# Optimization experiments

Hardware: AMD Instinct MI355X
Metric: run time of the kernel (lower is better)

The kernel has to match this reference:

```python
import jax, jax.numpy as jnp
import numpy as np

B, CIN, COUT, H, W = 4, 256, 256, 64, 64
K, G = 3, 4
PAD = (K - 1) // 2


def setup_inputs() -> dict:
    key = jax.random.key(0)
    k0, k1, k2, k3 = jax.random.split(key, 4)
    x = jax.random.normal(k0, (B, CIN, H, W), jnp.float32)
    y = jax.random.normal(k1, (B, 2, H, W), jnp.float32)
    # conv_offset: 1x1 conv, no bias, init std=0.1 (normal_init)
    w_offset = jax.random.normal(k2, (G * 2 * K * K, 2, 1, 1), jnp.float32) * 0.1
    # DeformConv2d weight, no bias, init std=0.01
    w_deform = jax.random.normal(k3, (COUT, CIN, K, K), jnp.float32) * 0.01
    return {"x": x, "y": y, "w_offset": w_offset, "w_deform": w_deform}


def _deform_conv(x, offset, weight):
    """DCN v1: stride 1, dilation 1, zero padding PAD, deform_groups=G, groups=1."""
    KK = K * K
    # mmcv offset layout: [B, G*2*KK, H, W] -> per group, per kernel pos, (dy, dx)
    off = offset.reshape(B, G, KK, 2, H, W)
    dy, dx = off[:, :, :, 0], off[:, :, :, 1]            # [B,G,KK,H,W]
    ii, jj = jnp.meshgrid(jnp.arange(K), jnp.arange(K), indexing="ij")
    ky = ii.reshape(KK).astype(x.dtype)                  # kernel row offsets
    kx = jj.reshape(KK).astype(x.dtype)                  # kernel col offsets
    base_y = jnp.arange(H, dtype=x.dtype)[None, :, None] - PAD + ky[:, None, None]  # [KK,H,1]
    base_x = jnp.arange(W, dtype=x.dtype)[None, None, :] - PAD + kx[:, None, None]  # [KK,1,W]
    yc = dy + base_y                                     # [B,G,KK,H,W]
    xc = dx + base_x

    Cg = CIN // G
    xg = x.reshape(B, G, Cg, H, W)

    def sample(xg1, yc1, xc1):
        # xg1 [Cg,H,W]; yc1/xc1 [KK,H,W] -> bilinear sample with zero padding
        y0 = jnp.floor(yc1)
        x0 = jnp.floor(xc1)
        wy = yc1 - y0
        wx = xc1 - x0
        y0i = y0.astype(jnp.int32)
        x0i = x0.astype(jnp.int32)

        def gather(yi, xi):
            valid = (yi >= 0) & (yi < H) & (xi >= 0) & (xi < W)
            v = xg1[:, jnp.clip(yi, 0, H - 1), jnp.clip(xi, 0, W - 1)]  # [Cg,KK,H,W]
            return v * valid[None].astype(xg1.dtype)

        v00 = gather(y0i, x0i)
        v01 = gather(y0i, x0i + 1)
        v10 = gather(y0i + 1, x0i)
        v11 = gather(y0i + 1, x0i + 1)
        return (v00 * (1 - wy) * (1 - wx) + v01 * (1 - wy) * wx
                + v10 * wy * (1 - wx) + v11 * wy * wx)

    sampled = jax.vmap(jax.vmap(sample))(xg, yc, xc)     # [B,G,Cg,KK,H,W]
    sampled = sampled.reshape(B, CIN, KK, H, W)
    wflat = weight.reshape(COUT, CIN, KK)
    return jnp.einsum("bckhw,ock->bohw", sampled, wflat)  # [B,COUT,H,W]


def reference(x, y, w_offset, w_deform):
    # offset = conv_offset(y.detach()), a 1x1 conv without bias
    y_det = jax.lax.stop_gradient(y)
    offset = jnp.einsum("bihw,oi->bohw", y_det, w_offset[:, :, 0, 0])
    out = _deform_conv(x, offset, w_deform)
    return jax.nn.relu(out)
```

## Files before the change

### kernel.cpp

```cpp
#include <hip/hip_runtime.h>
#include <cstddef>

#define B_    4
#define CIN_  256
#define COUT_ 256
#define H_    64
#define W_    64
#define KK_   9
#define G_    4
#define PAD_  1
#define TP    32

typedef short bf16x8 __attribute__((ext_vector_type(8)));
typedef float f32x4  __attribute__((ext_vector_type(4)));
typedef __attribute__((address_space(1))) const unsigned int* gptr_t;
typedef __attribute__((address_space(3))) unsigned int*       lptr_t;

__device__ __forceinline__ unsigned short f2bf(float v) {
    unsigned int u = __float_as_uint(v);
    u += 0x7fffu + ((u >> 16) & 1u);
    return (unsigned short)(u >> 16);
}
__device__ __forceinline__ float f_lo(unsigned int u) { return __uint_as_float(u << 16); }
__device__ __forceinline__ float f_hi(unsigned int u) { return __uint_as_float(u & 0xffff0000u); }

__global__ __launch_bounds__(256) void xt_kernel(const float* __restrict__ x,
                                                 unsigned short* __restrict__ xT) {
    __shared__ unsigned short s[128][66];
    const int tid   = threadIdx.x;
    const int bh    = blockIdx.x >> 1;
    const int chalf = blockIdx.x & 1;
    const size_t src_base = ((size_t)(bh >> 6) * CIN_ + chalf * 128) * (H_ * W_) + (bh & 63) * W_;
    #pragma unroll 4
    for (int k = 0; k < 32; ++k) {
        int i = k * 256 + tid;
        int c = i >> 6, w = i & 63;
        s[c][w] = f2bf(x[src_base + (size_t)c * (H_ * W_) + w]);
    }
    __syncthreads();
    #pragma unroll 4
    for (int k = 0; k < 16; ++k) {
        int j  = k * 256 + tid;
        int c2 = (j & 63) * 2, w = j >> 6;
        unsigned int lo = s[c2][w], hi = s[c2 + 1][w];
        *(unsigned int*)(xT + ((size_t)bh * 64 + w) * 256 + chalf * 128 + c2) = lo | (hi << 16);
    }
}

__global__ __launch_bounds__(256) void wt_kernel(const float* __restrict__ w,
                                                 unsigned short* __restrict__ wb) {
    int idx = blockIdx.x * 256 + threadIdx.x;
    int e   = idx & 7;
    int pos = (idx >> 3) & 7;
    int o   = (idx >> 6) & 255;
    int t   = idx >> 14;
    int g   = t / 9, kk = t - g * 9;
    int j   = pos ^ (o & 7);
    int c   = g * 64 + j * 8 + e;
    wb[idx] = f2bf(w[(o * CIN_ + c) * KK_ + kk]);
}

__global__ __launch_bounds__(256, 2) void dcn_kernel(
    const unsigned short* __restrict__ xT, const float* __restrict__ y,
    const float* __restrict__ w_off, const unsigned short* __restrict__ wb,
    float* __restrict__ out)
{
    __shared__ unsigned short s_W[COUT_ * 64];
    __shared__ unsigned short s_S[TP * 64];
    __shared__ float          s_off[72 * TP];

    const int tid = threadIdx.x;
    const int bid = blockIdx.x;
    const int xcd = bid & 7, loc = bid >> 3;
    const int b   = xcd >> 1;
    const int h   = (xcd & 1) * 32 + (loc >> 1);
    const int w0  = (loc & 1) * TP;

    for (int i = tid; i < 72 * TP; i += 256) {
        int p = i & 31, ch = i >> 5;
        float yv0 = y[((b * 2 + 0) * H_ + h) * W_ + w0 + p];
        float yv1 = y[((b * 2 + 1) * H_ + h) * W_ + w0 + p];
        s_off[i] = fmaf(yv0, w_off[ch * 2], yv1 * w_off[ch * 2 + 1]);
    }

    const int sp   = tid & 31;
    const int c8   = tid >> 5;
    const int lane = tid & 63, wave = tid >> 6;
    const int nt   = wave & 1, mh = wave >> 1;
    const int l15  = lane & 15, kq = lane >> 4, sw = l15 & 7;

    f32x4 acc[8];
    #pragma unroll
    for (int i = 0; i < 8; ++i) acc[i] = (f32x4){0.f, 0.f, 0.f, 0.f};

    for (int g = 0; g < G_; ++g) {
        for (int kk = 0; kk < KK_; ++kk) {
            const int step = g * KK_ + kk;
            __syncthreads();

            const unsigned short* src = wb + (size_t)step * 16384;
            #pragma unroll
            for (int j = 0; j < 8; ++j) {
                const int off = (j * 256 + tid) * 8;
                __builtin_amdgcn_global_load_lds((gptr_t)(src + off),
                                                 (lptr_t)(s_W + off), 16, 0, 0);
            }

            {
                const int   chy = step * 2;
                const float dy  = s_off[chy * 32 + sp];
                const float dx  = s_off[chy * 32 + 32 + sp];
                const float yc  = (float)(h + (kk / 3) - PAD_) + dy;
                const float xc  = (float)(w0 + sp + (kk % 3) - PAD_) + dx;
                const float yf  = floorf(yc), xf = floorf(xc);
                const float wy  = yc - yf,    wx = xc - xf;
                const int   yi  = (int)yf,    xi = (int)xf;
                float w00 = (1.f - wy) * (1.f - wx);
                float w01 = (1.f - wy) * wx;
                float w10 = wy * (1.f - wx);
                float w11 = wy * wx;
                const bool y0ok = (yi >= 0) & (yi < H_);
                const bool y1ok = (yi >= -1) & (yi < H_ - 1);
                const bool x0ok = (xi >= 0) & (xi < W_);
                const bool x1ok = (xi >= -1) & (xi < W_ - 1);
                w00 = (y0ok & x0ok) ? w00 : 0.f;
                w01 = (y0ok & x1ok) ? w01 : 0.f;
                w10 = (y1ok & x0ok) ? w10 : 0.f;
                w11 = (y1ok & x1ok) ? w11 : 0.f;
                const int y0c = min(max(yi, 0), H_ - 1);
                const int y1c = min(max(yi + 1, 0), H_ - 1);
                const int x0c = min(max(xi, 0), W_ - 1);
                const int x1c = min(max(xi + 1, 0), W_ - 1);
                const unsigned short* xb = xT + g * 64 + c8 * 8;
                const size_t bb = (size_t)b * (H_ * W_ * 256);
                const uint4 A = *(const uint4*)(xb + bb + ((size_t)y0c * W_ + x0c) * 256);
                const uint4 Bv= *(const uint4*)(xb + bb + ((size_t)y0c * W_ + x1c) * 256);
                const uint4 C = *(const uint4*)(xb + bb + ((size_t)y1c * W_ + x0c) * 256);
                const uint4 D = *(const uint4*)(xb + bb + ((size_t)y1c * W_ + x1c) * 256);
                const unsigned int av[4] = {A.x, A.y, A.z, A.w};
                const unsigned int bv[4] = {Bv.x, Bv.y, Bv.z, Bv.w};
                const unsigned int cv[4] = {C.x, C.y, C.z, C.w};
                const unsigned int dv[4] = {D.x, D.y, D.z, D.w};
                unsigned int res[4];
                #pragma unroll
                for (int q = 0; q < 4; ++q) {
                    float rl = w00 * f_lo(av[q]);
                    rl = fmaf(w01, f_lo(bv[q]), rl);
                    rl = fmaf(w10, f_lo(cv[q]), rl);
                    rl = fmaf(w11, f_lo(dv[q]), rl);
                    float rh = w00 * f_hi(av[q]);
                    rh = fmaf(w01, f_hi(bv[q]), rh);
                    rh = fmaf(w10, f_hi(cv[q]), rh);
                    rh = fmaf(w11, f_hi(dv[q]), rh);
                    res[q] = __builtin_amdgcn_perm(__float_as_uint(rh),
                                                   __float_as_uint(rl), 0x07060302u);
                }
                *(uint4*)(s_S + sp * 64 + ((c8 ^ (sp & 7)) * 8)) =
                    make_uint4(res[0], res[1], res[2], res[3]);
            }

            __syncthreads();

            const unsigned short* sSrow = s_S + (nt * 16 + l15) * 64;
            #pragma unroll
            for (int kh = 0; kh < 2; ++kh) {
                const int pos = ((kh * 4 + kq) ^ sw) * 8;
                const bf16x8 bfrag = *(const bf16x8*)(sSrow + pos);
                #pragma unroll
                for (int mt = 0; mt < 8; ++mt) {
                    const bf16x8 afrag =
                        *(const bf16x8*)(s_W + (mh * 128 + mt * 16 + l15) * 64 + pos);
                    acc[mt] = __builtin_amdgcn_mfma_f32_16x16x32_bf16(afrag, bfrag, acc[mt], 0, 0, 0);
                }
            }
        }
    }

    const int pxg = w0 + nt * 16 + l15;
    #pragma unroll
    for (int mt = 0; mt < 8; ++mt) {
        const int obase = mh * 128 + mt * 16 + kq * 4;
        #pragma unroll
        for (int r = 0; r < 4; ++r) {
            out[(((size_t)b * COUT_ + obase + r) * H_ + h) * W_ + pxg] =
                fmaxf(acc[mt][r], 0.f);
        }
    }
}

extern "C" void kernel_launch(void* const* d_in, const int* in_sizes, int n_in,
                              void* d_out, int out_size, void* d_ws, size_t ws_size,
                              hipStream_t stream) {
    const float* x     = (const float*)d_in[0];
    const float* y     = (const float*)d_in[1];
    const float* w_off = (const float*)d_in[2];
    const float* w_def = (const float*)d_in[3];
    float* out = (float*)d_out;

    unsigned short* xT = (unsigned short*)d_ws;
    unsigned short* wb = (unsigned short*)d_ws + 4194304;

    xt_kernel<<<B_ * H_ * 2, 256, 0, stream>>>(x, xT);
    wt_kernel<<<(KK_ * G_ * 64 * COUT_ * 8) / 256 / 8, 256, 0, stream>>>(w_def, wb);
    dcn_kernel<<<512, 256, 0, stream>>>(xT, y, w_off, wb, out);
}
```

Before: 137.9 us.

## Double-buffer weight and sample tiles with full-row 512-thread blocks

Each block now covers a full 64-pixel row with 512 threads instead of a half row with 256. Both the weight slice and the sampled-activation tile are double-buffered in LDS. The next step's weight DMA and bilinear gather are issued before the current step's MFMAs, which cuts the barriers per step from two to one and lets gather latency overlap compute. Offsets are now computed in registers from a float4 read of the offset weights, replacing the precomputed shared-memory offset table, and each weight slice is reused across twice as many pixels. The cost is more LDS per block (about 80KB) and only 256 blocks, so there is one block per CU and less latency hiding across blocks.

```diff
diff --git a/kernel.cpp b/kernel.cpp
--- a/kernel.cpp
+++ b/kernel.cpp
@@ -9,7 +9,8 @@
 #define KK_   9
 #define G_    4
 #define PAD_  1
-#define TP    32
+#define TPX   64
+#define NSTEP 36
 
 typedef short bf16x8 __attribute__((ext_vector_type(8)));
 typedef float f32x4  __attribute__((ext_vector_type(4)));
@@ -60,130 +61,141 @@
     wb[idx] = f2bf(w[(o * CIN_ + c) * KK_ + kk]);
 }
 
-__global__ __launch_bounds__(256, 2) void dcn_kernel(
+__global__ __launch_bounds__(512, 2) void dcn_kernel(
     const unsigned short* __restrict__ xT, const float* __restrict__ y,
     const float* __restrict__ w_off, const unsigned short* __restrict__ wb,
     float* __restrict__ out)
 {
-    __shared__ unsigned short s_W[COUT_ * 64];
-    __shared__ unsigned short s_S[TP * 64];
-    __shared__ float          s_off[72 * TP];
+    __shared__ unsigned short s_W[2][COUT_ * 64];
+    __shared__ unsigned short s_S[2][TPX * 64];
 
     const int tid = threadIdx.x;
     const int bid = blockIdx.x;
     const int xcd = bid & 7, loc = bid >> 3;
     const int b   = xcd >> 1;
-    const int h   = (xcd & 1) * 32 + (loc >> 1);
-    const int w0  = (loc & 1) * TP;
-
-    for (int i = tid; i < 72 * TP; i += 256) {
-        int p = i & 31, ch = i >> 5;
-        float yv0 = y[((b * 2 + 0) * H_ + h) * W_ + w0 + p];
-        float yv1 = y[((b * 2 + 1) * H_ + h) * W_ + w0 + p];
-        s_off[i] = fmaf(yv0, w_off[ch * 2], yv1 * w_off[ch * 2 + 1]);
-    }
-
-    const int sp   = tid & 31;
-    const int c8   = tid >> 5;
+    const int h   = (xcd & 1) * 32 + loc;
+
+    const int sp = tid & 63;
+    const int c8 = tid >> 6;
+
+    const float yv0 = y[((b * 2 + 0) * H_ + h) * W_ + sp];
+    const float yv1 = y[((b * 2 + 1) * H_ + h) * W_ + sp];
+
     const int lane = tid & 63, wave = tid >> 6;
-    const int nt   = wave & 1, mh = wave >> 1;
-    const int l15  = lane & 15, kq = lane >> 4, sw = l15 & 7;
+    const int pg  = wave & 1, oh = wave >> 1;
+    const int l15 = lane & 15, kq = lane >> 4, sw = l15 & 7;
 
     f32x4 acc[8];
     #pragma unroll
     for (int i = 0; i < 8; ++i) acc[i] = (f32x4){0.f, 0.f, 0.f, 0.f};
 
-    for (int g = 0; g < G_; ++g) {
-        for (int kk = 0; kk < KK_; ++kk) {
-            const int step = g * KK_ + kk;
-            __syncthreads();
-
-            const unsigned short* src = wb + (size_t)step * 16384;
+    const size_t xbase = (size_t)b * (H_ * W_ * 256) + c8 * 8;
+
+    auto dma_w = [&](int s, int buf) {
+        const unsigned short* src = wb + (size_t)s * 16384;
+        unsigned short* dst = &s_W[buf][0];
+        #pragma unroll
+        for (int j = 0; j < 4; ++j) {
+            const int off = (j * 512 + tid) * 8;
+            __builtin_amdgcn_global_load_lds((gptr_t)(src + off),
+                                             (lptr_t)(dst + off), 16, 0, 0);
+        }
+    };
+
+    auto sample = [&](int s, int buf) {
+        const int g  = s / 9;
+        const int kk = s - g * 9;
+        const float4 co = *(const float4*)(w_off + s * 4);
+        const float dy = fmaf(yv0, co.x, yv1 * co.y);
+        const float dx = fmaf(yv0, co.z, yv1 * co.w);
+        const float yc = (float)(h + (kk / 3) - PAD_) + dy;
+        const float xc = (float)(sp + (kk % 3) - PAD_) + dx;
+        const float yf = floorf(yc), xf = floorf(xc);
+        const float wy = yc - yf,    wx = xc - xf;
+        const int   yi = (int)yf,    xi = (int)xf;
+        float w00 = (1.f - wy) * (1.f - wx);
+        float w01 = (1.f - wy) * wx;
+        float w10 = wy * (1.f - wx);
+        float w11 = wy * wx;
+        const bool y0ok = (yi >= 0) & (yi < H_);
+        const bool y1ok = (yi >= -1) & (yi < H_ - 1);
+        const bool x0ok = (xi >= 0) & (xi < W_);
+        const bool x1ok = (xi >= -1) & (xi < W_ - 1);
+        w00 = (y0ok & x0ok) ? w00 : 0.f;
+        w01 = (y0ok & x1ok) ? w01 : 0.f;
+        w10 = (y1ok & x0ok) ? w10 : 0.f;
+        w11 = (y1ok & x1ok) ? w11 : 0.f;
+        const int y0c = min(max(yi, 0), H_ - 1);
+        const int y1c = min(max(yi + 1, 0), H_ - 1);
+        const int x0c = min(max(xi, 0), W_ - 1);
+        const int x1c = min(max(xi + 1, 0), W_ - 1);
+        const unsigned short* xb = xT + xbase + g * 64;
+        const uint4 A  = *(const uint4*)(xb + ((size_t)y0c * W_ + x0c) * 256);
+        const uint4 Bv = *(const uint4*)(xb + ((size_t)y0c * W_ + x1c) * 256);
+        const uint4 C  = *(const uint4*)(xb + ((size_t)y1c * W_ + x0c) * 256);
+        const uint4 D  = *(const uint4*)(xb + ((size_t)y1c * W_ + x1c) * 256);
+        const unsigned int av[4] = {A.x, A.y, A.z, A.w};
+        const unsigned int bv[4] = {Bv.x, Bv.y, Bv.z, Bv.w};
+        const unsigned int cv[4] = {C.x, C.y, C.z, C.w};
+        const unsigned int dv[4] = {D.x, D.y, D.z, D.w};
+        unsigned int res[4];
+        #pragma unroll
+        for (int q = 0; q < 4; ++q) {
+            float rl = w00 * f_lo(av[q]);
+            rl = fmaf(w01, f_lo(bv[q]), rl);
+            rl = fmaf(w10, f_lo(cv[q]), rl);
+            rl = fmaf(w11, f_lo(dv[q]), rl);
+            float rh = w00 * f_hi(av[q]);
+            rh = fmaf(w01, f_hi(bv[q]), rh);
+            rh = fmaf(w10, f_hi(cv[q]), rh);
+            rh = fmaf(w11, f_hi(dv[q]), rh);
+            res[q] = __builtin_amdgcn_perm(__float_as_uint(rh),
+                                           __float_as_uint(rl), 0x07060302u);
+        }
+        *(uint4*)(&s_S[buf][0] + sp * 64 + ((c8 ^ (sp & 7)) * 8)) =
+            make_uint4(res[0], res[1], res[2], res[3]);
+    };
+
+    dma_w(0, 0);
+    sample(0, 0);
+    __syncthreads();
+
+    for (int s = 0; s < NSTEP; ++s) {
+        const int cur = s & 1;
+        if (s < NSTEP - 1) {
+            dma_w(s + 1, cur ^ 1);
+            sample(s + 1, cur ^ 1);
+        }
+        const unsigned short* Wb = &s_W[cur][0];
+        const unsigned short* Sb = &s_S[cur][0];
+        #pragma unroll
+        for (int kh = 0; kh < 2; ++kh) {
+            const int pos = ((kh * 4 + kq) ^ sw) * 8;
             #pragma unroll
-            for (int j = 0; j < 8; ++j) {
-                const int off = (j * 256 + tid) * 8;
-                __builtin_amdgcn_global_load_lds((gptr_t)(src + off),
-                                                 (lptr_t)(s_W + off), 16, 0, 0);
-            }
-
-            {
-                const int   chy = step * 2;
-                const float dy  = s_off[chy * 32 + sp];
-                const float dx  = s_off[chy * 32 + 32 + sp];
-                const float yc  = (float)(h + (kk / 3) - PAD_) + dy;
-                const float xc  = (float)(w0 + sp + (kk % 3) - PAD_) + dx;
-                const float yf  = floorf(yc), xf = floorf(xc);
-                const float wy  = yc - yf,    wx = xc - xf;
-                const int   yi  = (int)yf,    xi = (int)xf;
-                float w00 = (1.f - wy) * (1.f - wx);
-                float w01 = (1.f - wy) * wx;
-                float w10 = wy * (1.f - wx);
-                float w11 = wy * wx;
-                const bool y0ok = (yi >= 0) & (yi < H_);
-                const bool y1ok = (yi >= -1) & (yi < H_ - 1);
-                const bool x0ok = (xi >= 0) & (xi < W_);
-                const bool x1ok = (xi >= -1) & (xi < W_ - 1);
-                w00 = (y0ok & x0ok) ? w00 : 0.f;
-                w01 = (y0ok & x1ok) ? w01 : 0.f;
-                w10 = (y1ok & x0ok) ? w10 : 0.f;
-                w11 = (y1ok & x1ok) ? w11 : 0.f;
-                const int y0c = min(max(yi, 0), H_ - 1);
-                const int y1c = min(max(yi + 1, 0), H_ - 1);
-                const int x0c = min(max(xi, 0), W_ - 1);
-                const int x1c = min(max(xi + 1, 0), W_ - 1);
-                const unsigned short* xb = xT + g * 64 + c8 * 8;
-                const size_t bb = (size_t)b * (H_ * W_ * 256);
-                const uint4 A = *(const uint4*)(xb + bb + ((size_t)y0c * W_ + x0c) * 256);
-                const uint4 Bv= *(const uint4*)(xb + bb + ((size_t)y0c * W_ + x1c) * 256);
-                const uint4 C = *(const uint4*)(xb + bb + ((size_t)y1c * W_ + x0c) * 256);
-                const uint4 D = *(const uint4*)(xb + bb + ((size_t)y1c * W_ + x1c) * 256);
-                const unsigned int av[4] = {A.x, A.y, A.z, A.w};
-                const unsigned int bv[4] = {Bv.x, Bv.y, Bv.z, Bv.w};
-                const unsigned int cv[4] = {C.x, C.y, C.z, C.w};
-                const unsigned int dv[4] = {D.x, D.y, D.z, D.w};
-                unsigned int res[4];
+            for (int nt = 0; nt < 2; ++nt) {
+                const bf16x8 bfrag = *(const bf16x8*)(Sb + (pg * 32 + nt * 16 + l15) * 64 + pos);
                 #pragma unroll
-                for (int q = 0; q < 4; ++q) {
-                    float rl = w00 * f_lo(av[q]);
-                    rl = fmaf(w01, f_lo(bv[q]), rl);
-                    rl = fmaf(w10, f_lo(cv[q]), rl);
-                    rl = fmaf(w11, f_lo(dv[q]), rl);
-                    float rh = w00 * f_hi(av[q]);
-                    rh = fmaf(w01, f_hi(bv[q]), rh);
-                    rh = fmaf(w10, f_hi(cv[q]), rh);
-                    rh = fmaf(w11, f_hi(dv[q]), rh);
-                    res[q] = __builtin_amdgcn_perm(__float_as_uint(rh),
-                                                   __float_as_uint(rl), 0x07060302u);
-                }
-                *(uint4*)(s_S + sp * 64 + ((c8 ^ (sp & 7)) * 8)) =
-                    make_uint4(res[0], res[1], res[2], res[3]);
-            }
-
-            __syncthreads();
-
-            const unsigned short* sSrow = s_S + (nt * 16 + l15) * 64;
-            #pragma unroll
-            for (int kh = 0; kh < 2; ++kh) {
-                const int pos = ((kh * 4 + kq) ^ sw) * 8;
-                const bf16x8 bfrag = *(const bf16x8*)(sSrow + pos);
-                #pragma unroll
-                for (int mt = 0; mt < 8; ++mt) {
-                    const bf16x8 afrag =
-                        *(const bf16x8*)(s_W + (mh * 128 + mt * 16 + l15) * 64 + pos);
-                    acc[mt] = __builtin_amdgcn_mfma_f32_16x16x32_bf16(afrag, bfrag, acc[mt], 0, 0, 0);
+                for (int mt = 0; mt < 4; ++mt) {
+                    const bf16x8 afrag = *(const bf16x8*)(Wb + (oh * 64 + mt * 16 + l15) * 64 + pos);
+                    acc[nt * 4 + mt] =
+                        __builtin_amdgcn_mfma_f32_16x16x32_bf16(afrag, bfrag, acc[nt * 4 + mt], 0, 0, 0);
                 }
             }
         }
-    }
-
-    const int pxg = w0 + nt * 16 + l15;
+        __syncthreads();
+    }
+
     #pragma unroll
-    for (int mt = 0; mt < 8; ++mt) {
-        const int obase = mh * 128 + mt * 16 + kq * 4;
-        #pragma unroll
-        for (int r = 0; r < 4; ++r) {
-            out[(((size_t)b * COUT_ + obase + r) * H_ + h) * W_ + pxg] =
-                fmaxf(acc[mt][r], 0.f);
+    for (int nt = 0; nt < 2; ++nt) {
+        const int px = pg * 32 + nt * 16 + l15;
+        #pragma unroll
+        for (int mt = 0; mt < 4; ++mt) {
+            const int obase = oh * 64 + mt * 16 + kq * 4;
+            #pragma unroll
+            for (int r = 0; r < 4; ++r) {
+                out[(((size_t)b * COUT_ + obase + r) * H_ + h) * W_ + px] =
+                    fmaxf(acc[nt * 4 + mt][r], 0.f);
+            }
         }
     }
 }
@@ -201,6 +213,6 @@
     unsigned short* wb = (unsigned short*)d_ws + 4194304;
 
     xt_kernel<<<B_ * H_ * 2, 256, 0, stream>>>(x, xT);
-    wt_kernel<<<(KK_ * G_ * 64 * COUT_ * 8) / 256 / 8, 256, 0, stream>>>(w_def, wb);
-    dcn_kernel<<<512, 256, 0, stream>>>(xT, y, w_off, wb, out);
-}
+    wt_kernel<<<(NSTEP * 16384) / 256, 256, 0, stream>>>(w_def, wb);
+    dcn_kernel<<<256, 512, 0, stream>>>(xT, y, w_off, wb, out);
+}
```

Result: slower. 147.6 us (+7.0%).
